# Optimization experiments

Hardware: AMD Instinct MI355X
Metric: run time of the kernel (lower is better)

Reference implementation:

```python
import jax, jax.numpy as jnp
import numpy as np

# BERT-base dims; 768 and max_sent_num=64 come from the module/config.
N, S, V, D, L, H, F = 8, 512, 30522, 768, 12, 12, 3072
DH = D // H
MAX_SENT = 64
LN_EPS = 1e-12
SCALE = float(np.sqrt(DH))


def _ln(x, g, b):
    m = jnp.mean(x, axis=-1, keepdims=True)
    v = jnp.mean(jnp.square(x - m), axis=-1, keepdims=True)
    return (x - m) * jax.lax.rsqrt(v + LN_EPS) * g + b


def setup_inputs() -> dict:
    key = jax.random.key(0)
    ks = jax.random.split(key, 10)
    # random token ids in a range avoiding the special ids 102/103
    ids = jax.random.randint(ks[0], (N, S), 999, 30000, dtype=jnp.int32)
    # variable per-doc sentence region -> ragged number of [MASK](103) separators (8..64)
    cutoff = jax.random.randint(ks[1], (N, 1), 64, S + 1)
    pos = jnp.arange(S)[None, :]
    sent_pos = ((pos % 8) == 7) & (pos < cutoff)
    ids = jnp.where(sent_pos, 103, ids)
    ids = ids.at[:, 0].set(102)  # exactly one [SEP]=102 per doc (required by the slice-assign)
    amask = jnp.ones((N, S), dtype=jnp.int32)
    g = lambda k, shape: 0.02 * jax.random.normal(k, shape, dtype=jnp.float32)
    inp = dict(input_ids_bert=ids, attention_mask_bert=amask)
    inp["tok_emb"] = g(ks[2], (V, D))
    inp["pos_emb"] = g(ks[3], (S, D))
    inp["emb_ln_g"] = jnp.ones((D,), jnp.float32)
    inp["emb_ln_b"] = jnp.zeros((D,), jnp.float32)
    inp["Wqkv"] = g(ks[4], (L, D, 3 * D))
    inp["bqkv"] = jnp.zeros((L, 3 * D), jnp.float32)
    inp["Wo"] = g(ks[5], (L, D, D))
    inp["bo"] = jnp.zeros((L, D), jnp.float32)
    inp["ln1_g"] = jnp.ones((L, D), jnp.float32)
    inp["ln1_b"] = jnp.zeros((L, D), jnp.float32)
    inp["W1"] = g(ks[6], (L, D, F))
    inp["b1"] = jnp.zeros((L, F), jnp.float32)
    inp["W2"] = g(ks[7], (L, F, D))
    inp["b2"] = jnp.zeros((L, D), jnp.float32)
    inp["ln2_g"] = jnp.ones((L, D), jnp.float32)
    inp["ln2_b"] = jnp.zeros((L, D), jnp.float32)
    return inp


def _bert(ids, amask, tok_emb, pos_emb, emb_ln_g, emb_ln_b,
          Wqkv, bqkv, Wo, bo, ln1_g, ln1_b, W1, b1, W2, b2, ln2_g, ln2_b):
    x = tok_emb[ids] + pos_emb[None, :, :]            # [N,S,D]
    x = _ln(x, emb_ln_g, emb_ln_b)
    bias = (1.0 - amask[:, None, None, :].astype(x.dtype)) * -1e9  # [N,1,1,S]

    def layer(x, p):
        wqkv, bq, wo, bo_, g1, b1n, w1, b1f, w2, b2f, g2, b2n = p
        qkv = x @ wqkv + bq
        q, k, v = jnp.split(qkv, 3, axis=-1)
        q = q.reshape(N, S, H, DH)
        k = k.reshape(N, S, H, DH)
        v = v.reshape(N, S, H, DH)
        att = jnp.einsum('bqhd,bkhd->bhqk', q, k) / SCALE + bias
        att = jax.nn.softmax(att, axis=-1)
        o = jnp.einsum('bhqk,bkhd->bqhd', att, v).reshape(N, S, D)
        x2 = _ln(x + o @ wo + bo_, g1, b1n)
        h = jax.nn.gelu(x2 @ w1 + b1f, approximate=False)
        return _ln(x2 + h @ w2 + b2f, g2, b2n), None

    x, _ = jax.lax.scan(layer, x, (Wqkv, bqkv, Wo, bo, ln1_g, ln1_b, W1, b1, W2, b2, ln2_g, ln2_b))
    return x


def _gather_scatter(ids, h):
    # Vectorized form of the per-doc python loop:
    #   out[doc, :n_sent] = concat([cls_emb(102), sent_embs(103)])[:-1]
    mask_sent = ids == 103
    mask_cls = ids == 102
    n_cls = mask_cls.sum(axis=1, keepdims=True)              # == 1 per doc
    total_sent = mask_sent.sum(axis=1, keepdims=True)        # ragged count
    rank_sent = jnp.cumsum(mask_sent, axis=1) - 1
    rank_cls = jnp.cumsum(mask_cls, axis=1) - 1
    dest = jnp.where(mask_cls, rank_cls,
                     jnp.where(mask_sent, n_cls + rank_sent, MAX_SENT))
    valid = (mask_cls | mask_sent) & (dest < total_sent) & (dest < MAX_SENT)
    dest_safe = jnp.where(valid, dest, MAX_SENT)             # dump invalid into scratch row
    vals = jnp.where(valid[..., None], h, 0.0)
    out = jnp.zeros((ids.shape[0], MAX_SENT + 1, D), dtype=h.dtype)
    out = out.at[jnp.arange(ids.shape[0])[:, None], dest_safe].set(vals)
    return out[:, :MAX_SENT]


def reference(input_ids_bert, attention_mask_bert, tok_emb, pos_emb, emb_ln_g, emb_ln_b,
              Wqkv, bqkv, Wo, bo, ln1_g, ln1_b, W1, b1, W2, b2, ln2_g, ln2_b):
    h = _bert(input_ids_bert, attention_mask_bert, tok_emb, pos_emb, emb_ln_g, emb_ln_b,
              Wqkv, bqkv, Wo, bo, ln1_g, ln1_b, W1, b1, W2, b2, ln2_g, ln2_b)
    return _gather_scatter(input_ids_bert, h)
```

## Files before the change

kernel.cpp:

```cpp
#include <hip/hip_runtime.h>
#include <hip/hip_bf16.h>

#define DEV static __device__ __forceinline__

using short8 = __attribute__((ext_vector_type(8))) short;
using f32x4 = __attribute__((ext_vector_type(4))) float;

DEV short f2bf(float f) {
  union { float f; unsigned u; } x; x.f = f;
  unsigned r = x.u + 0x7fffu + ((x.u >> 16) & 1u);
  return (short)(r >> 16);
}

DEV void gload16(const void* g, void* lds) {
  __builtin_amdgcn_global_load_lds(
      (const __attribute__((address_space(1))) void*)g,
      (__attribute__((address_space(3))) void*)lds, 16, 0, 0);
}

__global__ __launch_bounds__(256) void transpose_all_k(
    const float* __restrict__ Wqkv, const float* __restrict__ Wo,
    const float* __restrict__ W1, const float* __restrict__ W2,
    short* __restrict__ wqkvT, short* __restrict__ woT,
    short* __restrict__ w1T, short* __restrict__ w2T)
{
  __shared__ short t[64][72];
  const int b = blockIdx.x, tid = threadIdx.x;
  const float* in; short* out; int K, N, tt, nt;
  if (b < 432)       { in = Wqkv; out = wqkvT; K = 768;  N = 2304; tt = b;        nt = 36; }
  else if (b < 576)  { in = Wo;   out = woT;   K = 768;  N = 768;  tt = b - 432;  nt = 12; }
  else if (b < 1152) { in = W1;   out = w1T;   K = 768;  N = 3072; tt = b - 576;  nt = 48; }
  else               { in = W2;   out = w2T;   K = 3072; N = 768;  tt = b - 1152; nt = 12; }
  const int n0 = (tt % nt) * 64, k0 = (tt / nt) * 64;
  #pragma unroll
  for (int p = 0; p < 4; ++p) {
    int r = p * 16 + (tid >> 4), c4 = tid & 15;
    float4 v = *reinterpret_cast<const float4*>(in + (size_t)(k0 + r) * N + n0 + c4 * 4);
    t[r][c4 * 4 + 0] = f2bf(v.x);
    t[r][c4 * 4 + 1] = f2bf(v.y);
    t[r][c4 * 4 + 2] = f2bf(v.z);
    t[r][c4 * 4 + 3] = f2bf(v.w);
  }
  __syncthreads();
  #pragma unroll
  for (int q = 0; q < 2; ++q) {
    int n = tid >> 2, kc = (tid & 3) + q * 4;
    short8 o;
    #pragma unroll
    for (int j = 0; j < 8; ++j) o[j] = t[kc * 8 + j][n];
    *reinterpret_cast<short8*>(out + (size_t)(n0 + n) * K + k0 + kc * 8) = o;
  }
}

template <int BM, int EPI>
__global__ __launch_bounds__(256) void gemm_bt(
    const short* __restrict__ A, const short* __restrict__ Bt,
    const float* __restrict__ bias, const float* __restrict__ resid,
    void* __restrict__ Cout, int M, int Nn, int K)
{
  constexpr int AW = BM / 64;
  constexpr int MI = BM / 32;
  __shared__ short As[BM * 32];
  __shared__ short Bs[128 * 32];
  const int tid = threadIdx.x, lane = tid & 63, w = tid >> 6;
  const int wr = w >> 1, wc = w & 1;
  const int l15 = lane & 15, l4 = lane >> 4;
  const int m0 = blockIdx.y * BM, n0 = blockIdx.x * 128;
  const int crow = lane >> 2, ccol = (lane & 3) * 8;

  f32x4 acc[MI][4] = {};

  for (int k0 = 0; k0 < K; k0 += 32) {
    #pragma unroll
    for (int s = 0; s < AW; ++s) {
      int c = w * AW + s;
      gload16(A + (size_t)(m0 + c * 16 + crow) * K + k0 + ccol, &As[c * 512]);
    }
    #pragma unroll
    for (int s = 0; s < 2; ++s) {
      int c = w * 2 + s;
      gload16(Bt + (size_t)(n0 + c * 16 + crow) * K + k0 + ccol, &Bs[c * 512]);
    }
    __syncthreads();

    short8 af[MI], bfr[4];
    #pragma unroll
    for (int i = 0; i < MI; ++i)
      af[i] = *reinterpret_cast<const short8*>(&As[(wr * (BM / 2) + i * 16 + l15) * 32 + l4 * 8]);
    #pragma unroll
    for (int j = 0; j < 4; ++j)
      bfr[j] = *reinterpret_cast<const short8*>(&Bs[(wc * 64 + j * 16 + l15) * 32 + l4 * 8]);
    #pragma unroll
    for (int i = 0; i < MI; ++i)
      #pragma unroll
      for (int j = 0; j < 4; ++j)
        acc[i][j] = __builtin_amdgcn_mfma_f32_16x16x32_bf16(af[i], bfr[j], acc[i][j], 0, 0, 0);
    __syncthreads();
  }

  #pragma unroll
  for (int i = 0; i < MI; ++i) {
    #pragma unroll
    for (int j = 0; j < 4; ++j) {
      #pragma unroll
      for (int r = 0; r < 4; ++r) {
        int row = m0 + wr * (BM / 2) + i * 16 + l4 * 4 + r;
        int col = n0 + wc * 64 + j * 16 + l15;
        float v = acc[i][j][r] + bias[col];
        if constexpr (EPI == 1) v = 0.5f * v * (1.0f + erff(v * 0.70710678118654752f));
        if constexpr (EPI == 2) {
          ((float*)Cout)[(size_t)row * Nn + col] = v + resid[(size_t)row * Nn + col];
        } else {
          ((short*)Cout)[(size_t)row * Nn + col] = f2bf(v);
        }
      }
    }
  }
}

__global__ __launch_bounds__(256) void attn_k(
    const short* __restrict__ qkv, const int* __restrict__ amask,
    short* __restrict__ out)
{
  __shared__ short Kl[64][72];
  __shared__ short Vt[64][68];
  __shared__ short Pl[4][16][72];
  const int b = blockIdx.z, h = blockIdx.y, qt = blockIdx.x;
  const int tid = threadIdx.x, lane = tid & 63, w = tid >> 6;
  const int l15 = lane & 15, l4 = lane >> 4;
  const int tok0 = b * 512;
  const int q0 = qt * 64 + w * 16;

  short8 qf[2];
  #pragma unroll
  for (int kk = 0; kk < 2; ++kk)
    qf[kk] = *reinterpret_cast<const short8*>(
        qkv + (size_t)(tok0 + q0 + l15) * 2304 + h * 64 + kk * 32 + l4 * 8);

  f32x4 oacc[4] = {};
  float mrow[4], lrow[4];
  #pragma unroll
  for (int r = 0; r < 4; ++r) { mrow[r] = -1e30f; lrow[r] = 0.f; }

  for (int kt0 = 0; kt0 < 512; kt0 += 64) {
    #pragma unroll
    for (int i = 0; i < 2; ++i) {
      int c = tid + i * 256;
      int r = c >> 3, dc = c & 7;
      short8 v = *reinterpret_cast<const short8*>(
          qkv + (size_t)(tok0 + kt0 + r) * 2304 + 768 + h * 64 + dc * 8);
      *reinterpret_cast<short8*>(&Kl[r][dc * 8]) = v;
    }
    #pragma unroll
    for (int i = 0; i < 2; ++i) {
      int c = tid + i * 256;
      int r = c >> 3, dc = c & 7;
      short8 v = *reinterpret_cast<const short8*>(
          qkv + (size_t)(tok0 + kt0 + r) * 2304 + 1536 + h * 64 + dc * 8);
      #pragma unroll
      for (int j = 0; j < 8; ++j) Vt[dc * 8 + j][r] = v[j];
    }
    __syncthreads();

    f32x4 sacc[4] = {};
    #pragma unroll
    for (int t = 0; t < 4; ++t) {
      #pragma unroll
      for (int kk = 0; kk < 2; ++kk) {
        short8 kf = *reinterpret_cast<const short8*>(&Kl[t * 16 + l15][kk * 32 + l4 * 8]);
        sacc[t] = __builtin_amdgcn_mfma_f32_16x16x32_bf16(qf[kk], kf, sacc[t], 0, 0, 0);
      }
    }
    float p[4][4];
    #pragma unroll
    for (int t = 0; t < 4; ++t) {
      int ktok = kt0 + t * 16 + l15;
      float biasv = amask[b * 512 + ktok] ? 0.f : -1e9f;
      #pragma unroll
      for (int r = 0; r < 4; ++r) p[t][r] = sacc[t][r] * 0.125f + biasv;
    }
    #pragma unroll
    for (int r = 0; r < 4; ++r) {
      float mx = fmaxf(fmaxf(p[0][r], p[1][r]), fmaxf(p[2][r], p[3][r]));
      #pragma unroll
      for (int s = 1; s <= 8; s <<= 1) mx = fmaxf(mx, __shfl_xor(mx, s, 64));
      float mnew = fmaxf(mrow[r], mx);
      float alpha = __expf(mrow[r] - mnew);
      mrow[r] = mnew;
      float sum = 0.f;
      #pragma unroll
      for (int t = 0; t < 4; ++t) { p[t][r] = __expf(p[t][r] - mnew); sum += p[t][r]; }
      #pragma unroll
      for (int s = 1; s <= 8; s <<= 1) sum += __shfl_xor(sum, s, 64);
      lrow[r] = lrow[r] * alpha + sum;
      #pragma unroll
      for (int t = 0; t < 4; ++t) oacc[t][r] *= alpha;
    }
    #pragma unroll
    for (int t = 0; t < 4; ++t)
      #pragma unroll
      for (int r = 0; r < 4; ++r)
        Pl[w][l4 * 4 + r][t * 16 + l15] = f2bf(p[t][r]);
    __syncthreads();
    #pragma unroll
    for (int kk = 0; kk < 2; ++kk) {
      short8 pf = *reinterpret_cast<const short8*>(&Pl[w][l15][kk * 32 + l4 * 8]);
      #pragma unroll
      for (int t = 0; t < 4; ++t) {
        const unsigned* vp = reinterpret_cast<const unsigned*>(&Vt[t * 16 + l15][0]);
        union { short8 s; unsigned u[4]; } vu;
        #pragma unroll
        for (int w2 = 0; w2 < 4; ++w2) vu.u[w2] = vp[kk * 16 + l4 * 4 + w2];
        oacc[t] = __builtin_amdgcn_mfma_f32_16x16x32_bf16(pf, vu.s, oacc[t], 0, 0, 0);
      }
    }
    __syncthreads();
  }

  #pragma unroll
  for (int t = 0; t < 4; ++t)
    #pragma unroll
    for (int r = 0; r < 4; ++r) {
      int tok = tok0 + q0 + l4 * 4 + r;
      int dh = t * 16 + l15;
      out[(size_t)tok * 768 + h * 64 + dh] = f2bf(oacc[t][r] / lrow[r]);
    }
}

__global__ __launch_bounds__(256) void ln_k(
    const float* __restrict__ y, const float* __restrict__ g, const float* __restrict__ be,
    float* __restrict__ xf, short* __restrict__ xb)
{
  const int t = blockIdx.x, tid = threadIdx.x;
  const float* row = y + (size_t)t * 768;
  float v[3], s = 0.f, ss = 0.f;
  #pragma unroll
  for (int i = 0; i < 3; ++i) { v[i] = row[tid + i * 256]; s += v[i]; ss += v[i] * v[i]; }
  __shared__ float red[4][2];
  #pragma unroll
  for (int m = 1; m <= 32; m <<= 1) { s += __shfl_xor(s, m, 64); ss += __shfl_xor(ss, m, 64); }
  int w = tid >> 6;
  if ((tid & 63) == 0) { red[w][0] = s; red[w][1] = ss; }
  __syncthreads();
  s = red[0][0] + red[1][0] + red[2][0] + red[3][0];
  ss = red[0][1] + red[1][1] + red[2][1] + red[3][1];
  float mean = s * (1.f / 768.f);
  float var = ss * (1.f / 768.f) - mean * mean;
  float rs = rsqrtf(var + 1e-12f);
  #pragma unroll
  for (int i = 0; i < 3; ++i) {
    int c = tid + i * 256;
    float o = (v[i] - mean) * rs * g[c] + be[c];
    xf[(size_t)t * 768 + c] = o;
    xb[(size_t)t * 768 + c] = f2bf(o);
  }
}

__global__ __launch_bounds__(256) void embed_ln_k(
    const int* __restrict__ ids, const float* __restrict__ tok_emb,
    const float* __restrict__ pos_emb, const float* __restrict__ g,
    const float* __restrict__ be, float* __restrict__ xf, short* __restrict__ xb)
{
  const int t = blockIdx.x, tid = threadIdx.x;
  const int id = ids[t], sp = t & 511;
  float v[3], s = 0.f, ss = 0.f;
  #pragma unroll
  for (int i = 0; i < 3; ++i) {
    int c = tid + i * 256;
    v[i] = tok_emb[(size_t)id * 768 + c] + pos_emb[(size_t)sp * 768 + c];
    s += v[i]; ss += v[i] * v[i];
  }
  __shared__ float red[4][2];
  #pragma unroll
  for (int m = 1; m <= 32; m <<= 1) { s += __shfl_xor(s, m, 64); ss += __shfl_xor(ss, m, 64); }
  int w = tid >> 6;
  if ((tid & 63) == 0) { red[w][0] = s; red[w][1] = ss; }
  __syncthreads();
  s = red[0][0] + red[1][0] + red[2][0] + red[3][0];
  ss = red[0][1] + red[1][1] + red[2][1] + red[3][1];
  float mean = s * (1.f / 768.f);
  float var = ss * (1.f / 768.f) - mean * mean;
  float rs = rsqrtf(var + 1e-12f);
  #pragma unroll
  for (int i = 0; i < 3; ++i) {
    int c = tid + i * 256;
    float o = (v[i] - mean) * rs * g[c] + be[c];
    xf[(size_t)t * 768 + c] = o;
    xb[(size_t)t * 768 + c] = f2bf(o);
  }
}

__global__ __launch_bounds__(512) void gather_k(
    const int* __restrict__ ids, const float* __restrict__ x, float* __restrict__ out)
{
  const int doc = blockIdx.x, tid = threadIdx.x;
  const int lane = tid & 63, w = tid >> 6;
  __shared__ int src[64];
  __shared__ int wave_sent[8];
  __shared__ int cls_pos;
  if (tid < 64) src[tid] = -1;
  if (tid == 0) cls_pos = 0x7fffffff;
  __syncthreads();

  const int id = ids[doc * 512 + tid];
  const bool is_sent = (id == 103);
  const unsigned long long m = __ballot(is_sent);
  if (lane == 0) wave_sent[w] = __popcll(m);
  if (id == 102) atomicMin(&cls_pos, tid);
  __syncthreads();

  int total = 0, prefix = 0;
  #pragma unroll
  for (int i = 0; i < 8; ++i) {
    int c = wave_sent[i];
    if (i < w) prefix += c;
    total += c;
  }
  if (is_sent) {
    unsigned long long lt = lane ? (~0ULL >> (64 - lane)) : 0ULL;
    int d = 1 + prefix + __popcll(m & lt);
    if (d < total && d < 64) src[d] = tid;
  }
  if (tid == 0 && total > 0 && cls_pos != 0x7fffffff) src[0] = cls_pos;
  __syncthreads();

  for (int i = tid; i < 64 * 192; i += 512) {
    int row = i / 192, c4 = i - row * 192;
    int sp = src[row];
    float4 v = make_float4(0.f, 0.f, 0.f, 0.f);
    if (sp >= 0)
      v = reinterpret_cast<const float4*>(x + (size_t)(doc * 512 + sp) * 768)[c4];
    reinterpret_cast<float4*>(out + (size_t)doc * 64 * 768)[i] = v;
  }
}

extern "C" void kernel_launch(void* const* d_in, const int* in_sizes, int n_in,
                              void* d_out, int out_size, void* d_ws, size_t ws_size,
                              hipStream_t stream)
{
  const int* ids = (const int*)d_in[0];
  const int* am = (const int*)d_in[1];
  const float* tok_emb = (const float*)d_in[2];
  const float* pos_emb = (const float*)d_in[3];
  const float* eg = (const float*)d_in[4];
  const float* eb = (const float*)d_in[5];
  const float* Wqkv = (const float*)d_in[6];
  const float* bqkv = (const float*)d_in[7];
  const float* Wo = (const float*)d_in[8];
  const float* bo = (const float*)d_in[9];
  const float* g1 = (const float*)d_in[10];
  const float* b1n = (const float*)d_in[11];
  const float* W1 = (const float*)d_in[12];
  const float* b1f = (const float*)d_in[13];
  const float* W2 = (const float*)d_in[14];
  const float* b2f = (const float*)d_in[15];
  const float* g2 = (const float*)d_in[16];
  const float* b2n = (const float*)d_in[17];

  char* ws = (char*)d_ws;
  float* x_f   = (float*)(ws);
  short* x_b   = (short*)(ws + 12582912);
  float* x2_f  = (float*)(ws + 18874368);
  short* x2_b  = (short*)(ws + 31457280);
  float* y_f   = (float*)(ws + 37748736);
  short* qkv   = (short*)(ws + 50331648);
  short* attn  = (short*)(ws + 69206016);
  short* hb    = (short*)(ws + 75497472);
  short* wqkvT = (short*)(ws + 100663296);
  short* woT   = (short*)(ws + 104202240);
  short* w1T   = (short*)(ws + 105381888);
  short* w2T   = (short*)(ws + 110100480);

  embed_ln_k<<<4096, 256, 0, stream>>>(ids, tok_emb, pos_emb, eg, eb, x_f, x_b);

  for (int l = 0; l < 12; ++l) {
    transpose_all_k<<<1728, 256, 0, stream>>>(
        Wqkv + (size_t)l * 768 * 2304, Wo + (size_t)l * 768 * 768,
        W1 + (size_t)l * 768 * 3072, W2 + (size_t)l * 3072 * 768,
        wqkvT, woT, w1T, w2T);

    gemm_bt<128, 0><<<dim3(18, 32), 256, 0, stream>>>(
        x_b, wqkvT, bqkv + (size_t)l * 2304, nullptr, qkv, 4096, 2304, 768);
    attn_k<<<dim3(8, 12, 8), 256, 0, stream>>>(qkv, am, attn);
    gemm_bt<64, 2><<<dim3(6, 64), 256, 0, stream>>>(
        attn, woT, bo + (size_t)l * 768, x_f, y_f, 4096, 768, 768);
    ln_k<<<4096, 256, 0, stream>>>(y_f, g1 + (size_t)l * 768, b1n + (size_t)l * 768, x2_f, x2_b);
    gemm_bt<128, 1><<<dim3(24, 32), 256, 0, stream>>>(
        x2_b, w1T, b1f + (size_t)l * 3072, nullptr, hb, 4096, 3072, 768);
    gemm_bt<64, 2><<<dim3(6, 64), 256, 0, stream>>>(
        hb, w2T, b2f + (size_t)l * 768, x2_f, y_f, 4096, 768, 3072);
    ln_k<<<4096, 256, 0, stream>>>(y_f, g2 + (size_t)l * 768, b2n + (size_t)l * 768, x_f, x_b);
  }

  gather_k<<<8, 512, 0, stream>>>(ids, x_f, (float*)d_out);
}
```

Baseline: 2.428 ms.

## Split-K the N=768 output GEMMs and fold bias/residual reduction into LayerNorm

The Wo and W2 projections (N=768) now run as a 2-way split-K GEMM with 128x128 tiles, writing two fp32 partial buffers, instead of a 64-row tile GEMM with a fused bias+residual epilogue. A new LayerNorm kernel sums the two partials, adds bias and residual, then normalizes. The intent is to raise the block count and per-block reuse on the narrow GEMMs so the GPU is better filled. In exchange it writes an extra fp32 partial buffer, which reuses the qkv and hidden-activation scratch regions, and adds more read traffic in the LayerNorm.

```diff
diff --git a/kernel.cpp b/kernel.cpp
--- a/kernel.cpp
+++ b/kernel.cpp
@@ -108,14 +108,67 @@
         int col = n0 + wc * 64 + j * 16 + l15;
         float v = acc[i][j][r] + bias[col];
         if constexpr (EPI == 1) v = 0.5f * v * (1.0f + erff(v * 0.70710678118654752f));
-        if constexpr (EPI == 2) {
-          ((float*)Cout)[(size_t)row * Nn + col] = v + resid[(size_t)row * Nn + col];
-        } else {
-          ((short*)Cout)[(size_t)row * Nn + col] = f2bf(v);
-        }
+        ((short*)Cout)[(size_t)row * Nn + col] = f2bf(v);
       }
     }
   }
+}
+
+__global__ __launch_bounds__(256) void gemm_sk(
+    const short* __restrict__ A, const short* __restrict__ Bt,
+    float* __restrict__ p0, float* __restrict__ p1,
+    int M, int Nn, int Kstride, int Klen)
+{
+  __shared__ short As[128 * 32];
+  __shared__ short Bs[128 * 32];
+  const int tid = threadIdx.x, lane = tid & 63, w = tid >> 6;
+  const int wr = w >> 1, wc = w & 1;
+  const int l15 = lane & 15, l4 = lane >> 4;
+  const int m0 = blockIdx.y * 128, n0 = blockIdx.x * 128;
+  const int koff = blockIdx.z * Klen;
+  const int crow = lane >> 2, ccol = (lane & 3) * 8;
+
+  f32x4 acc[4][4] = {};
+
+  for (int k0 = 0; k0 < Klen; k0 += 32) {
+    #pragma unroll
+    for (int s = 0; s < 2; ++s) {
+      int c = w * 2 + s;
+      gload16(A + (size_t)(m0 + c * 16 + crow) * Kstride + koff + k0 + ccol, &As[c * 512]);
+    }
+    #pragma unroll
+    for (int s = 0; s < 2; ++s) {
+      int c = w * 2 + s;
+      gload16(Bt + (size_t)(n0 + c * 16 + crow) * Kstride + koff + k0 + ccol, &Bs[c * 512]);
+    }
+    __syncthreads();
+
+    short8 af[4], bfr[4];
+    #pragma unroll
+    for (int i = 0; i < 4; ++i)
+      af[i] = *reinterpret_cast<const short8*>(&As[(wr * 64 + i * 16 + l15) * 32 + l4 * 8]);
+    #pragma unroll
+    for (int j = 0; j < 4; ++j)
+      bfr[j] = *reinterpret_cast<const short8*>(&Bs[(wc * 64 + j * 16 + l15) * 32 + l4 * 8]);
+    #pragma unroll
+    for (int i = 0; i < 4; ++i)
+      #pragma unroll
+      for (int j = 0; j < 4; ++j)
+        acc[i][j] = __builtin_amdgcn_mfma_f32_16x16x32_bf16(af[i], bfr[j], acc[i][j], 0, 0, 0);
+    __syncthreads();
+  }
+
+  float* P = blockIdx.z ? p1 : p0;
+  #pragma unroll
+  for (int i = 0; i < 4; ++i)
+    #pragma unroll
+    for (int j = 0; j < 4; ++j)
+      #pragma unroll
+      for (int r = 0; r < 4; ++r) {
+        int row = m0 + wr * 64 + i * 16 + l4 * 4 + r;
+        int col = n0 + wc * 64 + j * 16 + l15;
+        P[(size_t)row * Nn + col] = acc[i][j][r];
+      }
 }
 
 __global__ __launch_bounds__(256) void attn_k(
@@ -227,15 +280,21 @@
     }
 }
 
-__global__ __launch_bounds__(256) void ln_k(
-    const float* __restrict__ y, const float* __restrict__ g, const float* __restrict__ be,
+__global__ __launch_bounds__(256) void ln2_k(
+    const float* __restrict__ p0, const float* __restrict__ p1,
+    const float* __restrict__ bias, const float* __restrict__ resid,
+    const float* __restrict__ g, const float* __restrict__ be,
     float* __restrict__ xf, short* __restrict__ xb)
 {
   const int t = blockIdx.x, tid = threadIdx.x;
-  const float* row = y + (size_t)t * 768;
+  const size_t base = (size_t)t * 768;
   float v[3], s = 0.f, ss = 0.f;
   #pragma unroll
-  for (int i = 0; i < 3; ++i) { v[i] = row[tid + i * 256]; s += v[i]; ss += v[i] * v[i]; }
+  for (int i = 0; i < 3; ++i) {
+    int c = tid + i * 256;
+    v[i] = p0[base + c] + p1[base + c] + bias[c] + resid[base + c];
+    s += v[i]; ss += v[i] * v[i];
+  }
   __shared__ float red[4][2];
   #pragma unroll
   for (int m = 1; m <= 32; m <<= 1) { s += __shfl_xor(s, m, 64); ss += __shfl_xor(ss, m, 64); }
@@ -251,8 +310,8 @@
   for (int i = 0; i < 3; ++i) {
     int c = tid + i * 256;
     float o = (v[i] - mean) * rs * g[c] + be[c];
-    xf[(size_t)t * 768 + c] = o;
-    xb[(size_t)t * 768 + c] = f2bf(o);
+    xf[base + c] = o;
+    xb[base + c] = f2bf(o);
   }
 }
 
@@ -364,8 +423,10 @@
   short* x2_b  = (short*)(ws + 31457280);
   float* y_f   = (float*)(ws + 37748736);
   short* qkv   = (short*)(ws + 50331648);
+  float* skp1b = (float*)(ws + 50331648);
   short* attn  = (short*)(ws + 69206016);
   short* hb    = (short*)(ws + 75497472);
+  float* skp1a = (float*)(ws + 75497472);
   short* wqkvT = (short*)(ws + 100663296);
   short* woT   = (short*)(ws + 104202240);
   short* w1T   = (short*)(ws + 105381888);
@@ -382,14 +443,21 @@
     gemm_bt<128, 0><<<dim3(18, 32), 256, 0, stream>>>(
         x_b, wqkvT, bqkv + (size_t)l * 2304, nullptr, qkv, 4096, 2304, 768);
     attn_k<<<dim3(8, 12, 8), 256, 0, stream>>>(qkv, am, attn);
-    gemm_bt<64, 2><<<dim3(6, 64), 256, 0, stream>>>(
-        attn, woT, bo + (size_t)l * 768, x_f, y_f, 4096, 768, 768);
-    ln_k<<<4096, 256, 0, stream>>>(y_f, g1 + (size_t)l * 768, b1n + (size_t)l * 768, x2_f, x2_b);
+
+    gemm_sk<<<dim3(6, 32, 2), 256, 0, stream>>>(
+        attn, woT, y_f, skp1a, 4096, 768, 768, 384);
+    ln2_k<<<4096, 256, 0, stream>>>(
+        y_f, skp1a, bo + (size_t)l * 768, x_f,
+        g1 + (size_t)l * 768, b1n + (size_t)l * 768, x2_f, x2_b);
+
     gemm_bt<128, 1><<<dim3(24, 32), 256, 0, stream>>>(
         x2_b, w1T, b1f + (size_t)l * 3072, nullptr, hb, 4096, 3072, 768);
-    gemm_bt<64, 2><<<dim3(6, 64), 256, 0, stream>>>(
-        hb, w2T, b2f + (size_t)l * 768, x2_f, y_f, 4096, 768, 3072);
-    ln_k<<<4096, 256, 0, stream>>>(y_f, g2 + (size_t)l * 768, b2n + (size_t)l * 768, x_f, x_b);
+
+    gemm_sk<<<dim3(6, 32, 2), 256, 0, stream>>>(
+        hb, w2T, y_f, skp1b, 4096, 768, 3072, 1536);
+    ln2_k<<<4096, 256, 0, stream>>>(
+        y_f, skp1b, b2f + (size_t)l * 768, x2_f,
+        g2 + (size_t)l * 768, b2n + (size_t)l * 768, x_f, x_b);
   }
 
   gather_k<<<8, 512, 0, stream>>>(ids, x_f, (float*)d_out);
```

Result: faster. 2.324 ms (-4.3%).

## Double-buffer GEMM K-loop and split-K the N=768 GEMMs into fused LN

Applied to the files above, without the earlier changes.

The GEMM main loop now stages 64-wide K tiles into two LDS buffers with async global-to-LDS loads, waiting on vmcnt so the next tile's loads overlap the current tile's MFMAs. The two N=768 GEMMs (attention output and FFN down) use 128-row tiles split two ways along K, each half writing a bf16 partial. Bias, residual add and the sum of the two partials move into a new fused layernorm kernel. This cuts global-memory stalls and raises block count for the narrow GEMMs, in exchange for more LDS per block, extra partial-sum traffic, and rounding both partials to bf16 before the residual add.

```diff
diff --git a/kernel.cpp b/kernel.cpp
--- a/kernel.cpp
+++ b/kernel.cpp
@@ -10,6 +10,11 @@
   union { float f; unsigned u; } x; x.f = f;
   unsigned r = x.u + 0x7fffu + ((x.u >> 16) & 1u);
   return (short)(r >> 16);
+}
+
+DEV float bf2f(short s) {
+  union { unsigned u; float f; } x; x.u = ((unsigned)(unsigned short)s) << 16;
+  return x.f;
 }
 
 DEV void gload16(const void* g, void* lds) {
@@ -55,47 +60,74 @@
 template <int BM, int EPI>
 __global__ __launch_bounds__(256) void gemm_bt(
     const short* __restrict__ A, const short* __restrict__ Bt,
-    const float* __restrict__ bias, const float* __restrict__ resid,
-    void* __restrict__ Cout, int M, int Nn, int K)
+    const float* __restrict__ bias,
+    void* __restrict__ C0, void* __restrict__ C1,
+    int M, int Nn, int Kstride, int Klen)
 {
   constexpr int AW = BM / 64;
   constexpr int MI = BM / 32;
-  __shared__ short As[BM * 32];
-  __shared__ short Bs[128 * 32];
+  constexpr int TA = BM * 64;
+  __shared__ short As[2 * TA];
+  __shared__ short Bs[2 * 128 * 64];
   const int tid = threadIdx.x, lane = tid & 63, w = tid >> 6;
   const int wr = w >> 1, wc = w & 1;
   const int l15 = lane & 15, l4 = lane >> 4;
   const int m0 = blockIdx.y * BM, n0 = blockIdx.x * 128;
+  const int koff = blockIdx.z * Klen;
   const int crow = lane >> 2, ccol = (lane & 3) * 8;
+  const int nt = Klen >> 6;
+
+  auto STAGE = [&](int q, int kt) {
+    const int k0 = koff + (kt << 6);
+    #pragma unroll
+    for (int ks = 0; ks < 2; ++ks) {
+      #pragma unroll
+      for (int s = 0; s < AW; ++s) {
+        int c = w * AW + s;
+        gload16(A + (size_t)(m0 + c * 16 + crow) * Kstride + k0 + ks * 32 + ccol,
+                &As[q * TA + ks * BM * 32 + c * 512]);
+      }
+      #pragma unroll
+      for (int s = 0; s < 2; ++s) {
+        int c = w * 2 + s;
+        gload16(Bt + (size_t)(n0 + c * 16 + crow) * Kstride + k0 + ks * 32 + ccol,
+                &Bs[q * 8192 + ks * 4096 + c * 512]);
+      }
+    }
+  };
+
+  STAGE(0, 0);
+  STAGE(1, 1);
 
   f32x4 acc[MI][4] = {};
 
-  for (int k0 = 0; k0 < K; k0 += 32) {
-    #pragma unroll
-    for (int s = 0; s < AW; ++s) {
-      int c = w * AW + s;
-      gload16(A + (size_t)(m0 + c * 16 + crow) * K + k0 + ccol, &As[c * 512]);
-    }
-    #pragma unroll
-    for (int s = 0; s < 2; ++s) {
-      int c = w * 2 + s;
-      gload16(Bt + (size_t)(n0 + c * 16 + crow) * K + k0 + ccol, &Bs[c * 512]);
-    }
-    __syncthreads();
-
-    short8 af[MI], bfr[4];
-    #pragma unroll
-    for (int i = 0; i < MI; ++i)
-      af[i] = *reinterpret_cast<const short8*>(&As[(wr * (BM / 2) + i * 16 + l15) * 32 + l4 * 8]);
-    #pragma unroll
-    for (int j = 0; j < 4; ++j)
-      bfr[j] = *reinterpret_cast<const short8*>(&Bs[(wc * 64 + j * 16 + l15) * 32 + l4 * 8]);
-    #pragma unroll
-    for (int i = 0; i < MI; ++i)
+  for (int kt = 0; kt < nt; ++kt) {
+    if (kt + 1 < nt) asm volatile("s_waitcnt vmcnt(8)" ::: "memory");
+    else             asm volatile("s_waitcnt vmcnt(0)" ::: "memory");
+    __builtin_amdgcn_s_barrier();
+    __builtin_amdgcn_sched_barrier(0);
+    const int q = kt & 1;
+    #pragma unroll
+    for (int ks = 0; ks < 2; ++ks) {
+      short8 af[MI], bfr[4];
+      #pragma unroll
+      for (int i = 0; i < MI; ++i)
+        af[i] = *reinterpret_cast<const short8*>(
+            &As[q * TA + ks * BM * 32 + (wr * (BM / 2) + i * 16 + l15) * 32 + l4 * 8]);
       #pragma unroll
       for (int j = 0; j < 4; ++j)
-        acc[i][j] = __builtin_amdgcn_mfma_f32_16x16x32_bf16(af[i], bfr[j], acc[i][j], 0, 0, 0);
-    __syncthreads();
+        bfr[j] = *reinterpret_cast<const short8*>(
+            &Bs[q * 8192 + ks * 4096 + (wc * 64 + j * 16 + l15) * 32 + l4 * 8]);
+      #pragma unroll
+      for (int i = 0; i < MI; ++i)
+        #pragma unroll
+        for (int j = 0; j < 4; ++j)
+          acc[i][j] = __builtin_amdgcn_mfma_f32_16x16x32_bf16(af[i], bfr[j], acc[i][j], 0, 0, 0);
+    }
+    __builtin_amdgcn_sched_barrier(0);
+    __builtin_amdgcn_s_barrier();
+    __builtin_amdgcn_sched_barrier(0);
+    if (kt + 2 < nt) STAGE(q, kt + 2);
   }
 
   #pragma unroll
@@ -106,12 +138,13 @@
       for (int r = 0; r < 4; ++r) {
         int row = m0 + wr * (BM / 2) + i * 16 + l4 * 4 + r;
         int col = n0 + wc * 64 + j * 16 + l15;
-        float v = acc[i][j][r] + bias[col];
-        if constexpr (EPI == 1) v = 0.5f * v * (1.0f + erff(v * 0.70710678118654752f));
-        if constexpr (EPI == 2) {
-          ((float*)Cout)[(size_t)row * Nn + col] = v + resid[(size_t)row * Nn + col];
+        if constexpr (EPI == 3) {
+          short* P = (short*)(blockIdx.z ? C1 : C0);
+          P[(size_t)row * Nn + col] = f2bf(acc[i][j][r]);
         } else {
-          ((short*)Cout)[(size_t)row * Nn + col] = f2bf(v);
+          float v = acc[i][j][r] + bias[col];
+          if constexpr (EPI == 1) v = 0.5f * v * (1.0f + erff(v * 0.70710678118654752f));
+          ((short*)C0)[(size_t)row * Nn + col] = f2bf(v);
         }
       }
     }
@@ -227,15 +260,21 @@
     }
 }
 
-__global__ __launch_bounds__(256) void ln_k(
-    const float* __restrict__ y, const float* __restrict__ g, const float* __restrict__ be,
+__global__ __launch_bounds__(256) void ln2_k(
+    const short* __restrict__ p0, const short* __restrict__ p1,
+    const float* __restrict__ bias, const float* __restrict__ resid,
+    const float* __restrict__ g, const float* __restrict__ be,
     float* __restrict__ xf, short* __restrict__ xb)
 {
   const int t = blockIdx.x, tid = threadIdx.x;
-  const float* row = y + (size_t)t * 768;
+  const size_t base = (size_t)t * 768;
   float v[3], s = 0.f, ss = 0.f;
   #pragma unroll
-  for (int i = 0; i < 3; ++i) { v[i] = row[tid + i * 256]; s += v[i]; ss += v[i] * v[i]; }
+  for (int i = 0; i < 3; ++i) {
+    int c = tid + i * 256;
+    v[i] = bf2f(p0[base + c]) + bf2f(p1[base + c]) + bias[c] + resid[base + c];
+    s += v[i]; ss += v[i] * v[i];
+  }
   __shared__ float red[4][2];
   #pragma unroll
   for (int m = 1; m <= 32; m <<= 1) { s += __shfl_xor(s, m, 64); ss += __shfl_xor(ss, m, 64); }
@@ -251,8 +290,8 @@
   for (int i = 0; i < 3; ++i) {
     int c = tid + i * 256;
     float o = (v[i] - mean) * rs * g[c] + be[c];
-    xf[(size_t)t * 768 + c] = o;
-    xb[(size_t)t * 768 + c] = f2bf(o);
+    xf[base + c] = o;
+    xb[base + c] = f2bf(o);
   }
 }
 
@@ -362,10 +401,12 @@
   short* x_b   = (short*)(ws + 12582912);
   float* x2_f  = (float*)(ws + 18874368);
   short* x2_b  = (short*)(ws + 31457280);
-  float* y_f   = (float*)(ws + 37748736);
+  short* skp0  = (short*)(ws + 37748736);
   short* qkv   = (short*)(ws + 50331648);
+  short* skp1b = (short*)(ws + 50331648);
   short* attn  = (short*)(ws + 69206016);
   short* hb    = (short*)(ws + 75497472);
+  short* skp1a = (short*)(ws + 75497472);
   short* wqkvT = (short*)(ws + 100663296);
   short* woT   = (short*)(ws + 104202240);
   short* w1T   = (short*)(ws + 105381888);
@@ -379,17 +420,24 @@
         W1 + (size_t)l * 768 * 3072, W2 + (size_t)l * 3072 * 768,
         wqkvT, woT, w1T, w2T);
 
-    gemm_bt<128, 0><<<dim3(18, 32), 256, 0, stream>>>(
-        x_b, wqkvT, bqkv + (size_t)l * 2304, nullptr, qkv, 4096, 2304, 768);
+    gemm_bt<128, 0><<<dim3(18, 32, 1), 256, 0, stream>>>(
+        x_b, wqkvT, bqkv + (size_t)l * 2304, qkv, nullptr, 4096, 2304, 768, 768);
     attn_k<<<dim3(8, 12, 8), 256, 0, stream>>>(qkv, am, attn);
-    gemm_bt<64, 2><<<dim3(6, 64), 256, 0, stream>>>(
-        attn, woT, bo + (size_t)l * 768, x_f, y_f, 4096, 768, 768);
-    ln_k<<<4096, 256, 0, stream>>>(y_f, g1 + (size_t)l * 768, b1n + (size_t)l * 768, x2_f, x2_b);
-    gemm_bt<128, 1><<<dim3(24, 32), 256, 0, stream>>>(
-        x2_b, w1T, b1f + (size_t)l * 3072, nullptr, hb, 4096, 3072, 768);
-    gemm_bt<64, 2><<<dim3(6, 64), 256, 0, stream>>>(
-        hb, w2T, b2f + (size_t)l * 768, x2_f, y_f, 4096, 768, 3072);
-    ln_k<<<4096, 256, 0, stream>>>(y_f, g2 + (size_t)l * 768, b2n + (size_t)l * 768, x_f, x_b);
+
+    gemm_bt<128, 3><<<dim3(6, 32, 2), 256, 0, stream>>>(
+        attn, woT, nullptr, skp0, skp1a, 4096, 768, 768, 384);
+    ln2_k<<<4096, 256, 0, stream>>>(
+        skp0, skp1a, bo + (size_t)l * 768, x_f,
+        g1 + (size_t)l * 768, b1n + (size_t)l * 768, x2_f, x2_b);
+
+    gemm_bt<128, 1><<<dim3(24, 32, 1), 256, 0, stream>>>(
+        x2_b, w1T, b1f + (size_t)l * 3072, hb, nullptr, 4096, 3072, 768, 768);
+
+    gemm_bt<128, 3><<<dim3(6, 32, 2), 256, 0, stream>>>(
+        hb, w2T, nullptr, skp0, skp1b, 4096, 768, 3072, 1536);
+    ln2_k<<<4096, 256, 0, stream>>>(
+        skp0, skp1b, b2f + (size_t)l * 768, x2_f,
+        g2 + (size_t)l * 768, b2n + (size_t)l * 768, x_f, x_b);
   }
 
   gather_k<<<8, 512, 0, stream>>>(ids, x_f, (float*)d_out);
```

New measurement: 2.250 ms. -7.3%, faster.
